# Optimization experiments

Hardware: AMD Instinct MI355X
Metric: run time of the kernel (lower is better)

## Reference

```python
import jax, jax.numpy as jnp
import numpy as np


def setup_inputs() -> dict:
    key = jax.random.key(0)
    k1, k2 = jax.random.split(key)
    B, T, D, P = 32, 8192, 128, 1024
    mel = jax.random.normal(k1, (B, T, D), dtype=jnp.float32)
    # durations in [0, 9); max possible sum = P*8 = T, so slices never overrun
    duration = jax.random.randint(k2, (B, P), 0, 9, dtype=jnp.int64)
    return {"mel": mel, "duration": duration}


def reference(mel, duration):
    # mel: (B, T, D) float; duration: (B, P) int, consumed sequentially.
    B, T, D = mel.shape
    P = duration.shape[1]
    ends = jnp.cumsum(duration, axis=1)  # (B, P): exclusive end frame of each phoneme
    t = jnp.arange(T)
    # segment id of frame t = first phoneme whose end > t; frames past sum(d) map to P
    seg = jax.vmap(lambda e: jnp.searchsorted(e, t, side="right"))(ends)  # (B, T)
    sums = jax.vmap(
        lambda m, s: jax.ops.segment_sum(m, s, num_segments=P + 1)
    )(mel, seg)[:, :P]  # (B, P, D), dropping the overflow bucket
    d = duration.astype(mel.dtype)[..., None]  # (B, P, 1)
    # mean over each phoneme's frames; zeros where duration == 0 (matches torch init)
    return jnp.where(d > 0, sums / jnp.maximum(d, 1), jnp.zeros((), mel.dtype))
```

## Files before the change

### kernel.cpp

```cpp
#include <hip/hip_runtime.h>

#define BB 32
#define TT 8192
#define DD 128
#define PP 1024

__global__ void __launch_bounds__(512)
phoneme_fused_kernel(const float* __restrict__ mel,
                     const int* __restrict__ dur,
                     float* __restrict__ out) {
    __shared__ int wave_tot[8];
    __shared__ int starts_sh[PP];
    __shared__ int dur_sh[PP];

    const int b      = blockIdx.x >> 6;
    const int pblk   = blockIdx.x & 63;
    const int t      = threadIdx.x;
    const int wave   = t >> 6;
    const int lane64 = t & 63;

    const int2 v = ((const int2*)(dur + b * PP))[t];
    const int tsum = v.x + v.y;

    int scan = tsum;
    #pragma unroll
    for (int off = 1; off < 64; off <<= 1) {
        int up = __shfl_up(scan, off, 64);
        if (lane64 >= off) scan += up;
    }
    if (lane64 == 63) wave_tot[wave] = scan;
    __syncthreads();

    int wave_prefix = 0;
    #pragma unroll
    for (int w = 0; w < 7; ++w) {
        int wt = wave_tot[w];
        if (w < wave) wave_prefix += wt;
    }

    const int excl = wave_prefix + (scan - tsum);
    starts_sh[2 * t]     = excl;
    starts_sh[2 * t + 1] = excl + v.x;
    dur_sh[2 * t]        = v.x;
    dur_sh[2 * t + 1]    = v.y;
    __syncthreads();

    const int r    = t >> 5;
    const int lane = t & 31;
    const int p    = pblk * 16 + r;

    const int s = starts_sh[p];
    const int d = dur_sh[p];

    const float4* base =
        (const float4*)(mel + ((size_t)b * TT + (size_t)s) * DD) + lane;

    float4 acc[8];
    #pragma unroll
    for (int k = 0; k < 8; ++k) {
        acc[k] = make_float4(0.f, 0.f, 0.f, 0.f);
        if (k < d) acc[k] = base[k * (DD / 4)];
    }

    #pragma unroll
    for (int off = 4; off >= 1; off >>= 1) {
        #pragma unroll
        for (int k = 0; k < off; ++k) {
            acc[k].x += acc[k + off].x;
            acc[k].y += acc[k + off].y;
            acc[k].z += acc[k + off].z;
            acc[k].w += acc[k + off].w;
        }
    }

    const float inv = (d > 0) ? (1.0f / (float)d) : 0.0f;
    acc[0].x *= inv; acc[0].y *= inv; acc[0].z *= inv; acc[0].w *= inv;

    ((float4*)out)[((size_t)b * PP + p) * (DD / 4) + lane] = acc[0];
}

extern "C" void kernel_launch(void* const* d_in, const int* in_sizes, int n_in,
                              void* d_out, int out_size, void* d_ws, size_t ws_size,
                              hipStream_t stream) {
    const float* mel = (const float*)d_in[0];
    const int*   dur = (const int*)d_in[1];
    float*       out = (float*)d_out;

    phoneme_fused_kernel<<<(BB * PP) / 16, 512, 0, stream>>>(mel, dur, out);
}
```

Measured before the change: 180.4 us.

## Split fused kernel into per-batch scan plus separate averaging kernel

```diff
diff --git a/kernel.cpp b/kernel.cpp
--- a/kernel.cpp
+++ b/kernel.cpp
@@ -6,15 +6,10 @@
 #define PP 1024
 
 __global__ void __launch_bounds__(512)
-phoneme_fused_kernel(const float* __restrict__ mel,
-                     const int* __restrict__ dur,
-                     float* __restrict__ out) {
+phoneme_scan_kernel(const int* __restrict__ dur, int4* __restrict__ seg) {
     __shared__ int wave_tot[8];
-    __shared__ int starts_sh[PP];
-    __shared__ int dur_sh[PP];
 
-    const int b      = blockIdx.x >> 6;
-    const int pblk   = blockIdx.x & 63;
+    const int b      = blockIdx.x;
     const int t      = threadIdx.x;
     const int wave   = t >> 6;
     const int lane64 = t & 63;
@@ -39,18 +34,20 @@
     }
 
     const int excl = wave_prefix + (scan - tsum);
-    starts_sh[2 * t]     = excl;
-    starts_sh[2 * t + 1] = excl + v.x;
-    dur_sh[2 * t]        = v.x;
-    dur_sh[2 * t + 1]    = v.y;
-    __syncthreads();
+    seg[b * (PP / 2) + t] = make_int4(excl, v.x, excl + v.x, v.y);
+}
 
-    const int r    = t >> 5;
-    const int lane = t & 31;
-    const int p    = pblk * 16 + r;
+__global__ void __launch_bounds__(256)
+phoneme_avg_kernel(const float* __restrict__ mel,
+                   const int2* __restrict__ seg,
+                   float* __restrict__ out) {
+    const int row  = (blockIdx.x << 3) + (threadIdx.x >> 5);
+    const int lane = threadIdx.x & 31;
+    const int b    = row >> 10;
 
-    const int s = starts_sh[p];
-    const int d = dur_sh[p];
+    const int2 sd = seg[row];
+    const int s = sd.x;
+    const int d = sd.y;
 
     const float4* base =
         (const float4*)(mel + ((size_t)b * TT + (size_t)s) * DD) + lane;
@@ -76,7 +73,7 @@
     const float inv = (d > 0) ? (1.0f / (float)d) : 0.0f;
     acc[0].x *= inv; acc[0].y *= inv; acc[0].z *= inv; acc[0].w *= inv;
 
-    ((float4*)out)[((size_t)b * PP + p) * (DD / 4) + lane] = acc[0];
+    ((float4*)out)[(size_t)row * (DD / 4) + lane] = acc[0];
 }
 
 extern "C" void kernel_launch(void* const* d_in, const int* in_sizes, int n_in,
@@ -85,6 +82,9 @@
     const float* mel = (const float*)d_in[0];
     const int*   dur = (const int*)d_in[1];
     float*       out = (float*)d_out;
+    int4*        seg = (int4*)d_ws;
 
-    phoneme_fused_kernel<<<(BB * PP) / 16, 512, 0, stream>>>(mel, dur, out);
+    phoneme_scan_kernel<<<BB, 512, 0, stream>>>(dur, seg);
+    phoneme_avg_kernel<<<(BB * PP) / 8, 256, 0, stream>>>(
+        mel, (const int2*)seg, out);
 }
```

Measured after the change: 181.6 us. About the same (+0.7%).
